# Performance work log

Measured on AMD Instinct MI355X. Metric: run time of the kernel, lower is better.

The kernel has to match this reference:

```python
import jax, jax.numpy as jnp
import numpy as np

D_MODEL = 4096
D_FIBER = 64
D_LATENT = 512
OMEGA = 0.1
B, L = 4, 4096


def cayley(A):
    # Q = (I - A)^{-1} (I + A), batched over leading dim; A is skew-symmetric
    d = A.shape[-1]
    I = jnp.eye(d, dtype=A.dtype)
    return jnp.linalg.solve(I - A, I + A)


def setup_inputs() -> dict:
    key = jax.random.key(0)
    k1, k2, k3, k4, k5 = jax.random.split(key, 5)
    h_t = jax.random.normal(k1, (B, L, D_MODEL), dtype=jnp.float32)
    z0 = jax.random.normal(k2, (B, D_LATENT), dtype=jnp.float32)
    A_raw = jax.random.normal(k3, (B, D_FIBER, D_FIBER), dtype=jnp.float32) * 0.1
    A_u = A_raw - jnp.swapaxes(A_raw, -1, -2)  # skew-symmetric gauge connection
    # frozen projection weights, torch nn.Linear layout: (out_features, in_features)
    W_down = jax.random.normal(k4, (D_FIBER, D_MODEL), dtype=jnp.float32) / np.sqrt(D_MODEL)
    W_up = jax.random.normal(k5, (D_MODEL, D_FIBER), dtype=jnp.float32) / np.sqrt(D_FIBER)
    alpha = jnp.float32(OMEGA)
    return {"h_t": h_t, "z0": z0, "A_u": A_u, "alpha": alpha, "W_down": W_down, "W_up": W_up}


def reference(h_t, z0, A_u, alpha, W_down, W_up):
    # psi_down: (B,L,d_model) @ (d_model,d_fiber)
    h_fiber = jnp.einsum('bld,fd->blf', h_t, W_down)
    Q_u = cayley(A_u)  # (B, d_fiber, d_fiber)
    # h_fiber @ Q_u^T per batch
    h_rot = jnp.einsum('blf,bgf->blg', h_fiber, Q_u)
    delta = h_rot - h_fiber
    h_out = h_t + alpha * jnp.einsum('blf,df->bld', delta, W_up)
    return h_out
```

## Files before the change

kernel.cpp:

```cpp
#include <hip/hip_runtime.h>
#include <hip/hip_bf16.h>

#define D_MODEL 4096
#define NFIB    64
#define NBATCH  4
#define LSEQ    4096

typedef __attribute__((ext_vector_type(4))) float f32x4;
typedef __attribute__((ext_vector_type(8))) short bf16x8;

__device__ __forceinline__ unsigned short f2bf(float f) {
  unsigned int u = __builtin_bit_cast(unsigned int, f);
  u += 0x7FFFu + ((u >> 16) & 1u);
  return (unsigned short)(u >> 16);
}

__device__ __forceinline__ bf16x8 cvt8(f32x4 a, f32x4 b) {
  union { __hip_bfloat162 h2[4]; bf16x8 v; } u;
  u.h2[0] = __float22bfloat162_rn(make_float2(a[0], a[1]));
  u.h2[1] = __float22bfloat162_rn(make_float2(a[2], a[3]));
  u.h2[2] = __float22bfloat162_rn(make_float2(b[0], b[1]));
  u.h2[3] = __float22bfloat162_rn(make_float2(b[2], b[3]));
  return u.v;
}

__global__ __launch_bounds__(256) void prep1_kernel(const float* __restrict__ A,
                                                    const float* __restrict__ Wd,
                                                    float* __restrict__ S,
                                                    unsigned short* __restrict__ Wd2) {
  const int blk = blockIdx.x;
  if (blk >= NBATCH) {
    int idx = (blk - NBATCH) * 256 + threadIdx.x;
    int j    = idx & 7;
    int lane = (idx >> 3) & 63;
    int nf   = (idx >> 9) & 3;
    int ks   = idx >> 11;
    int row = nf * 16 + (lane & 15);
    int col = ks * 32 + (lane >> 4) * 8 + j;
    Wd2[idx] = f2bf(Wd[row * D_MODEL + col]);
    return;
  }
  __shared__ float M[64][66];
  __shared__ float R[64][66];
  const int b = blk;
  const int tid = threadIdx.x;
  const int k = tid & 63;
  const int g = tid >> 6;
  const float* Ab = A + b * 4096;
#pragma unroll
  for (int ii = 0; ii < 16; ++ii) {
    int i = g * 16 + ii;
    float a = Ab[i * 64 + k];
    M[i][k] = ((i == k) ? 1.0f : 0.0f) - a;
    R[i][k] = 2.0f * a;
  }
  for (int j = 0; j < 64; ++j) {
    __syncthreads();
    float pr  = 1.0f / M[j][j];
    float mjk = M[j][k], rjk = R[j][k];
    float f[16];
#pragma unroll
    for (int ii = 0; ii < 16; ++ii) f[ii] = M[g * 16 + ii][j] * pr;
    __syncthreads();
#pragma unroll
    for (int ii = 0; ii < 16; ++ii) {
      int i = g * 16 + ii;
      if (i != j) { M[i][k] -= f[ii] * mjk; R[i][k] -= f[ii] * rjk; }
    }
  }
  __syncthreads();
  float* Sb = S + b * 4096;
#pragma unroll
  for (int ii = 0; ii < 16; ++ii) {
    int i = g * 16 + ii;
    Sb[i * 64 + k] = R[i][k] / M[i][i];
  }
}

__global__ __launch_bounds__(256) void prep_u_kernel(const float* __restrict__ Wup,
                                                     const float* __restrict__ S,
                                                     const float* __restrict__ alpha_p,
                                                     unsigned short* __restrict__ U2) {
  __shared__ float Sl[4096];
  const int blk = blockIdx.x;
  const int b = blk >> 7;
  const int ntg = blk & 127;
  const float* Sb = S + b * 4096;
  for (int i = threadIdx.x; i < 1024; i += 256)
    ((f32x4*)Sl)[i] = ((const f32x4*)Sb)[i];
  __syncthreads();

  const int t = threadIdx.x;
  const int nt   = ntg * 2 + (t >> 7);
  const int h    = (t >> 6) & 1;
  const int lane = t & 63;
  const int d = nt * 16 + (lane & 15);
  const int fbase = h * 32 + (lane >> 4) * 8;
  const float alpha = alpha_p[0];
  const f32x4* wr = (const f32x4*)(Wup + d * 64);

  float s[8];
#pragma unroll
  for (int j = 0; j < 8; ++j) s[j] = 0.f;
#pragma unroll
  for (int g4 = 0; g4 < 16; ++g4) {
    f32x4 wv = wr[g4];
#pragma unroll
    for (int gg = 0; gg < 4; ++gg) {
      const float* srow = &Sl[(g4 * 4 + gg) * 64 + fbase];
      float wvg = wv[gg];
#pragma unroll
      for (int j = 0; j < 8; ++j) s[j] += wvg * srow[j];
    }
  }
  bf16x8 v;
#pragma unroll
  for (int j = 0; j < 8; ++j) v[j] = (short)f2bf(alpha * s[j]);
  *(bf16x8*)(U2 + ((((size_t)b * 256 + nt) * 64 + lane) * 2 + h) * 8) = v;
}

__global__ __launch_bounds__(256, 8) void p1_kernel(
    const float* __restrict__ H, const unsigned short* __restrict__ Wd2,
    unsigned short* __restrict__ F2) {
  const int blk = blockIdx.x;
  const int row0 = blk * 16;
  const int tid = threadIdx.x;
  const int w = tid >> 6, l = tid & 63, lr = l & 15, lq = l >> 4;

  __shared__ float Hs[2 * 16 * 128];
  auto lds3 = (__attribute__((address_space(3))) char*)Hs;
  const char* hb = (const char*)(H + (size_t)row0 * D_MODEL);

  int srow[2], scc[2];
#pragma unroll
  for (int q = 0; q < 2; ++q) {
    int off = q * 4096 + tid * 16;
    srow[q] = off >> 9;
    scc[q]  = (off & 511) ^ ((srow[q] & 7) << 4);
  }

#define STAGE(KCH, BUF)                                                        \
  {                                                                            \
    _Pragma("unroll")                                                          \
    for (int q = 0; q < 2; ++q) {                                              \
      const char* g = hb + (size_t)srow[q] * 16384 + (KCH) * 512 + scc[q];     \
      __builtin_amdgcn_global_load_lds(                                        \
          (const __attribute__((address_space(1))) void*)g,                    \
          (__attribute__((address_space(3))) void*)(lds3 + (BUF) * 8192 +      \
                                                    q * 4096 + tid * 16),      \
          16, 0, 0);                                                           \
    }                                                                          \
  }

  f32x4 acc = {0, 0, 0, 0};
  const int abase = lr * 512;
  const int axor = (lr & 7) << 4;

  STAGE(0, 0);
  for (int kch = 0; kch < 32; ++kch) {
    const int buf = kch & 1;
    if (kch < 31) {
      STAGE(kch + 1, buf ^ 1);
      asm volatile("s_waitcnt vmcnt(2)" ::: "memory");
    } else {
      asm volatile("s_waitcnt vmcnt(0)" ::: "memory");
    }
    __builtin_amdgcn_s_barrier();
    __builtin_amdgcn_sched_barrier(0);
#pragma unroll
    for (int s = 0; s < 4; ++s) {
      const int coff = s * 128 + lq * 32;
      f32x4 h0 = *(const f32x4*)((const char*)Hs + buf * 8192 + abase + (coff ^ axor));
      f32x4 h1 = *(const f32x4*)((const char*)Hs + buf * 8192 + abase + ((coff + 16) ^ axor));
      bf16x8 bfr = *(const bf16x8*)(Wd2 + (((size_t)(kch * 4 + s) * 4 + w) * 64 + l) * 8);
      acc = __builtin_amdgcn_mfma_f32_16x16x32_bf16(cvt8(h0, h1), bfr, acc, 0, 0, 0);
    }
    __builtin_amdgcn_s_barrier();
  }
#undef STAGE

#pragma unroll
  for (int rr = 0; rr < 4; ++rr)
    F2[(size_t)(row0 + lq * 4 + rr) * 64 + w * 16 + lr] = f2bf(acc[rr]);
}

__global__ __launch_bounds__(256, 8) void p2_kernel(
    const float* __restrict__ H, const unsigned short* __restrict__ F2,
    const unsigned short* __restrict__ U2, float* __restrict__ Out) {
  const int blk = blockIdx.x;
  const int tile = blk >> 2;
  const int ch = blk & 3;
  const int row0 = tile * 16;
  const int b = tile >> 8;
  const int tid = threadIdx.x;
  const int w = tid >> 6, l = tid & 63, lr = l & 15, lq = l >> 4;

  const int cbase = ch * 1024 + w * 256;
  const int nt0 = cbase >> 4;

  bf16x8 fb0 = *(const bf16x8*)(F2 + (size_t)(row0 + lr) * 64 + lq * 8);
  bf16x8 fb1 = *(const bf16x8*)(F2 + (size_t)(row0 + lr) * 64 + 32 + lq * 8);

  const unsigned short* ub = U2 + (((size_t)b * 256 + nt0) * 64 + l) * 16;
  const size_t obase = (size_t)(row0 + lr) * D_MODEL + cbase + lq * 4;

  bf16x8 u0r[2], u1r[2];
  f32x4 hr[2];
#pragma unroll
  for (int q = 0; q < 2; ++q) {
    u0r[q] = *(const bf16x8*)(ub + q * 1024);
    u1r[q] = *(const bf16x8*)(ub + q * 1024 + 8);
    hr[q]  = *(const f32x4*)(H + obase + q * 16);
  }

#pragma unroll
  for (int nf = 0; nf < 16; ++nf) {
    __builtin_amdgcn_sched_barrier(0);
    f32x4 c = {0, 0, 0, 0};
    c = __builtin_amdgcn_mfma_f32_16x16x32_bf16(u0r[nf & 1], fb0, c, 0, 0, 0);
    c = __builtin_amdgcn_mfma_f32_16x16x32_bf16(u1r[nf & 1], fb1, c, 0, 0, 0);
    f32x4 v = hr[nf & 1] + c;
    *(f32x4*)(Out + obase + nf * 16) = v;
    if (nf + 2 < 16) {
      u0r[nf & 1] = *(const bf16x8*)(ub + (nf + 2) * 1024);
      u1r[nf & 1] = *(const bf16x8*)(ub + (nf + 2) * 1024 + 8);
      hr[nf & 1]  = *(const f32x4*)(H + obase + (nf + 2) * 16);
    }
    __builtin_amdgcn_sched_barrier(0);
  }
}

extern "C" void kernel_launch(void* const* d_in, const int* in_sizes, int n_in,
                              void* d_out, int out_size, void* d_ws, size_t ws_size,
                              hipStream_t stream) {
  const float* h_t    = (const float*)d_in[0];
  const float* A_u    = (const float*)d_in[2];
  const float* alpha  = (const float*)d_in[3];
  const float* W_down = (const float*)d_in[4];
  const float* W_up   = (const float*)d_in[5];
  float* out = (float*)d_out;

  char* ws = (char*)d_ws;
  float*          S   = (float*)ws;
  unsigned short* Wd2 = (unsigned short*)(ws + (64 << 10));
  unsigned short* U2  = (unsigned short*)(ws + (576 << 10));
  unsigned short* F2  = (unsigned short*)(ws + (2624 << 10));

  prep1_kernel<<<NBATCH + 1024, 256, 0, stream>>>(A_u, W_down, S, Wd2);
  prep_u_kernel<<<512, 256, 0, stream>>>(W_up, S, alpha, U2);
  p1_kernel<<<1024, 256, 0, stream>>>(h_t, Wd2, F2);
  p2_kernel<<<4096, 256, 0, stream>>>(h_t, F2, U2, out);
}
```

Measured before the change: 301.1 us.

## Replace LDS staging in p1 with direct batched global loads; batch p2 loads

The p1 down-projection drops its LDS double-buffered global_load_lds pipeline and the two barriers per step. Instead each lane reads its H fragments straight from global memory in batches of four k-steps before issuing the MFMAs. p2 replaces its rolling two-deep software prefetch with blocks of four loads followed by four MFMA pairs. Both kernels relax launch bounds from 8 to 4 waves per EU, which allows more registers. The aim is to cut barrier and LDS overhead, with the risk of less latency hiding and uncoalesced 32-byte-strided H reads in p1.

```diff
diff --git a/kernel.cpp b/kernel.cpp
--- a/kernel.cpp
+++ b/kernel.cpp
@@ -119,7 +119,7 @@
   *(bf16x8*)(U2 + ((((size_t)b * 256 + nt) * 64 + lane) * 2 + h) * 8) = v;
 }
 
-__global__ __launch_bounds__(256, 8) void p1_kernel(
+__global__ __launch_bounds__(256, 4) void p1_kernel(
     const float* __restrict__ H, const unsigned short* __restrict__ Wd2,
     unsigned short* __restrict__ F2) {
   const int blk = blockIdx.x;
@@ -127,64 +127,35 @@
   const int tid = threadIdx.x;
   const int w = tid >> 6, l = tid & 63, lr = l & 15, lq = l >> 4;
 
-  __shared__ float Hs[2 * 16 * 128];
-  auto lds3 = (__attribute__((address_space(3))) char*)Hs;
-  const char* hb = (const char*)(H + (size_t)row0 * D_MODEL);
-
-  int srow[2], scc[2];
-#pragma unroll
-  for (int q = 0; q < 2; ++q) {
-    int off = q * 4096 + tid * 16;
-    srow[q] = off >> 9;
-    scc[q]  = (off & 511) ^ ((srow[q] & 7) << 4);
-  }
-
-#define STAGE(KCH, BUF)                                                        \
-  {                                                                            \
-    _Pragma("unroll")                                                          \
-    for (int q = 0; q < 2; ++q) {                                              \
-      const char* g = hb + (size_t)srow[q] * 16384 + (KCH) * 512 + scc[q];     \
-      __builtin_amdgcn_global_load_lds(                                        \
-          (const __attribute__((address_space(1))) void*)g,                    \
-          (__attribute__((address_space(3))) void*)(lds3 + (BUF) * 8192 +      \
-                                                    q * 4096 + tid * 16),      \
-          16, 0, 0);                                                           \
-    }                                                                          \
-  }
+  const float* ha = H + (size_t)(row0 + lr) * D_MODEL + lq * 8;
+  const unsigned short* wb = Wd2 + ((size_t)w * 64 + l) * 8;
 
   f32x4 acc = {0, 0, 0, 0};
-  const int abase = lr * 512;
-  const int axor = (lr & 7) << 4;
-
-  STAGE(0, 0);
-  for (int kch = 0; kch < 32; ++kch) {
-    const int buf = kch & 1;
-    if (kch < 31) {
-      STAGE(kch + 1, buf ^ 1);
-      asm volatile("s_waitcnt vmcnt(2)" ::: "memory");
-    } else {
-      asm volatile("s_waitcnt vmcnt(0)" ::: "memory");
-    }
-    __builtin_amdgcn_s_barrier();
-    __builtin_amdgcn_sched_barrier(0);
-#pragma unroll
-    for (int s = 0; s < 4; ++s) {
-      const int coff = s * 128 + lq * 32;
-      f32x4 h0 = *(const f32x4*)((const char*)Hs + buf * 8192 + abase + (coff ^ axor));
-      f32x4 h1 = *(const f32x4*)((const char*)Hs + buf * 8192 + abase + ((coff + 16) ^ axor));
-      bf16x8 bfr = *(const bf16x8*)(Wd2 + (((size_t)(kch * 4 + s) * 4 + w) * 64 + l) * 8);
-      acc = __builtin_amdgcn_mfma_f32_16x16x32_bf16(cvt8(h0, h1), bfr, acc, 0, 0, 0);
-    }
-    __builtin_amdgcn_s_barrier();
-  }
-#undef STAGE
+
+  for (int sb = 0; sb < 32; ++sb) {
+    const float* hp = ha + sb * 128;
+    const unsigned short* wp = wb + (size_t)sb * 8192;
+    f32x4 a0[4], a1[4];
+    bf16x8 bfr[4];
+#pragma unroll
+    for (int u = 0; u < 4; ++u) {
+      a0[u] = *(const f32x4*)(hp + u * 32);
+      a1[u] = *(const f32x4*)(hp + u * 32 + 4);
+      bfr[u] = *(const bf16x8*)(wp + u * 2048);
+    }
+    __builtin_amdgcn_sched_barrier(0);
+#pragma unroll
+    for (int u = 0; u < 4; ++u)
+      acc = __builtin_amdgcn_mfma_f32_16x16x32_bf16(cvt8(a0[u], a1[u]), bfr[u], acc, 0, 0, 0);
+    __builtin_amdgcn_sched_barrier(0);
+  }
 
 #pragma unroll
   for (int rr = 0; rr < 4; ++rr)
     F2[(size_t)(row0 + lq * 4 + rr) * 64 + w * 16 + lr] = f2bf(acc[rr]);
 }
 
-__global__ __launch_bounds__(256, 8) void p2_kernel(
+__global__ __launch_bounds__(256, 4) void p2_kernel(
     const float* __restrict__ H, const unsigned short* __restrict__ F2,
     const unsigned short* __restrict__ U2, float* __restrict__ Out) {
   const int blk = blockIdx.x;
@@ -204,27 +175,24 @@
   const unsigned short* ub = U2 + (((size_t)b * 256 + nt0) * 64 + l) * 16;
   const size_t obase = (size_t)(row0 + lr) * D_MODEL + cbase + lq * 4;
 
-  bf16x8 u0r[2], u1r[2];
-  f32x4 hr[2];
-#pragma unroll
-  for (int q = 0; q < 2; ++q) {
-    u0r[q] = *(const bf16x8*)(ub + q * 1024);
-    u1r[q] = *(const bf16x8*)(ub + q * 1024 + 8);
-    hr[q]  = *(const f32x4*)(H + obase + q * 16);
-  }
-
-#pragma unroll
-  for (int nf = 0; nf < 16; ++nf) {
-    __builtin_amdgcn_sched_barrier(0);
-    f32x4 c = {0, 0, 0, 0};
-    c = __builtin_amdgcn_mfma_f32_16x16x32_bf16(u0r[nf & 1], fb0, c, 0, 0, 0);
-    c = __builtin_amdgcn_mfma_f32_16x16x32_bf16(u1r[nf & 1], fb1, c, 0, 0, 0);
-    f32x4 v = hr[nf & 1] + c;
-    *(f32x4*)(Out + obase + nf * 16) = v;
-    if (nf + 2 < 16) {
-      u0r[nf & 1] = *(const bf16x8*)(ub + (nf + 2) * 1024);
-      u1r[nf & 1] = *(const bf16x8*)(ub + (nf + 2) * 1024 + 8);
-      hr[nf & 1]  = *(const f32x4*)(H + obase + (nf + 2) * 16);
+  for (int nb = 0; nb < 4; ++nb) {
+    const unsigned short* up = ub + (size_t)nb * 4096;
+    const float* hp = H + obase + nb * 64;
+    bf16x8 u0r[4], u1r[4];
+    f32x4 hr[4];
+#pragma unroll
+    for (int u = 0; u < 4; ++u) {
+      u0r[u] = *(const bf16x8*)(up + u * 1024);
+      u1r[u] = *(const bf16x8*)(up + u * 1024 + 8);
+      hr[u]  = *(const f32x4*)(hp + u * 16);
+    }
+    __builtin_amdgcn_sched_barrier(0);
+#pragma unroll
+    for (int u = 0; u < 4; ++u) {
+      f32x4 c = {0, 0, 0, 0};
+      c = __builtin_amdgcn_mfma_f32_16x16x32_bf16(u0r[u], fb0, c, 0, 0, 0);
+      c = __builtin_amdgcn_mfma_f32_16x16x32_bf16(u1r[u], fb1, c, 0, 0, 0);
+      *(f32x4*)(Out + obase + (nb * 4 + u) * 16) = hr[u] + c;
     }
     __builtin_amdgcn_sched_barrier(0);
   }
```

Result: slower. 357.1 us (+18.6%).
